# Kernel tuning notes

Measured on AMD Instinct MI355X. Metric: run time of the kernel, lower is better.

The kernel has to match this reference:

```python
import jax, jax.numpy as jnp
import numpy as np

B, T, D = 2, 2048, 2048
H, HD = 16, 128
ROPE_BASE = 10000.0
EPS = 1e-6


def setup_inputs() -> dict:
    key = jax.random.key(0)
    ks = jax.random.split(key, 5)
    s = 1.0 / np.sqrt(D)
    return {
        "x": jax.random.normal(ks[0], (B, T, D), dtype=jnp.float32),
        "Wq": jax.random.normal(ks[1], (H * HD, D), dtype=jnp.float32) * s,
        "Wk": jax.random.normal(ks[2], (H * HD, D), dtype=jnp.float32) * s,
        "Wv": jax.random.normal(ks[3], (H * HD, D), dtype=jnp.float32) * s,
        "Wo": jax.random.normal(ks[4], (D, H * HD), dtype=jnp.float32) * s,
        "q_norm_w": jnp.ones((HD,), dtype=jnp.float32),
        "k_norm_w": jnp.ones((HD,), dtype=jnp.float32),
    }


def _rms_norm(x, w):
    # RMSNorm over last dim, no centering (LLaMA/Qwen style)
    norm = jnp.sqrt(jnp.mean(jnp.square(x), axis=-1, keepdims=True) + EPS)
    return x / norm * w


def _rope_interleaved(x):
    # x: (B, T, H, HD); GPT-NeoX interleaved style, sequential positions
    dim = HD // 2
    freqs = jnp.exp(-jnp.arange(0, dim, dtype=jnp.float32) * jnp.log(ROPE_BASE) / dim)
    angles = jnp.arange(T, dtype=jnp.float32)[:, None] * freqs[None, :]  # (T, dim)
    cos = jnp.cos(angles)[None, :, None, :]  # (1, T, 1, dim)
    sin = jnp.sin(angles)[None, :, None, :]
    x_even = x[..., ::2]
    x_odd = x[..., 1::2]
    r_even = x_even * cos - x_odd * sin
    r_odd = x_even * sin + x_odd * cos
    return jnp.stack([r_even, r_odd], axis=-1).reshape(x.shape)


def reference(x, Wq, Wk, Wv, Wo, q_norm_w, k_norm_w):
    # QKV projections (weights stored [out, in], per llm_linear einsum)
    q = jnp.einsum("btd,od->bto", x, Wq).reshape(B, T, H, HD)
    k = jnp.einsum("btd,od->bto", x, Wk).reshape(B, T, H, HD)
    v = jnp.einsum("btd,od->bto", x, Wv).reshape(B, T, H, HD)
    # per-head QK RMSNorm
    q = _rms_norm(q, q_norm_w)
    k = _rms_norm(k, k_norm_w)
    # rotary embeddings
    q = _rope_interleaved(q)
    k = _rope_interleaved(k)
    # causal scaled dot-product attention
    scale = 1.0 / jnp.sqrt(jnp.asarray(HD, dtype=x.dtype))
    scores = jnp.einsum("bthd,bshd->bhts", q, k) * scale  # (B, H, T, T)
    causal = jnp.tril(jnp.ones((T, T), dtype=bool))
    scores = jnp.where(causal[None, None, :, :], scores, jnp.asarray(-1e30, dtype=scores.dtype))
    probs = jax.nn.softmax(scores, axis=-1)
    ctx = jnp.einsum("bhts,bshd->bthd", probs, v).reshape(B, T, H * HD)
    # output projection
    return jnp.einsum("bto,do->btd", ctx, Wo)
```

## Files before the change

### kernel.cpp

```cpp
#include <hip/hip_runtime.h>
#include <cstdint>
#include <cstddef>

#define B_ 2
#define T_ 2048
#define D_ 2048
#define H_ 16
#define HD_ 128
#define EPS_ 1e-6f
#define QSCALE_ 0.08838834764831845f
#define KVSTRIDE_ (H_ * HD_)

typedef unsigned short u16;
typedef short s16x8 __attribute__((ext_vector_type(8)));
typedef float f32x4 __attribute__((ext_vector_type(4)));

__device__ __forceinline__ float bf2f(u16 h) {
  union { unsigned int u; float f; } v;
  v.u = ((unsigned int)h) << 16;
  return v.f;
}
__device__ __forceinline__ u16 f2bf(float f) {
  union { float f; unsigned int u; } v;
  v.f = f;
  unsigned int r = v.u + 0x7FFFu + ((v.u >> 16) & 1u);
  return (u16)(r >> 16);
}

__device__ __forceinline__ void gload16(const void* g, void* l) {
  __builtin_amdgcn_global_load_lds(
      (const __attribute__((address_space(1))) unsigned int*)g,
      (__attribute__((address_space(3))) unsigned int*)l, 16, 0, 0);
}

__global__ void cvt_f32_bf16(const float* __restrict__ in, u16* __restrict__ out, int n4) {
  int i = blockIdx.x * blockDim.x + threadIdx.x;
  if (i < n4) {
    float4 v = ((const float4*)in)[i];
    ((ushort4*)out)[i] = make_ushort4(f2bf(v.x), f2bf(v.y), f2bf(v.z), f2bf(v.w));
  }
}

template <int OUT_BF16>
__global__ __launch_bounds__(256, 2) void gemm_btn(const u16* __restrict__ A,
                                                   const u16* __restrict__ Bm,
                                                   void* __restrict__ Cout,
                                                   int M, int N, int K) {
  __shared__ u16 As[2 * 128 * 32];
  __shared__ u16 Bs[2 * 128 * 32];
  const int tid = threadIdx.x;
  const int w = tid >> 6, lane = tid & 63, quad = lane >> 4, c = lane & 15;
  const int wm = w & 1, wn = w >> 1;
  const int m0 = blockIdx.y * 128, n0 = blockIdx.x * 128;

  f32x4 acc[4][4];
#pragma unroll
  for (int i = 0; i < 4; ++i)
#pragma unroll
    for (int j = 0; j < 4; ++j) acc[i][j] = (f32x4){0.f, 0.f, 0.f, 0.f};

  for (int k0 = 0; k0 < K; k0 += 64) {
    __syncthreads();
#pragma unroll
    for (int i = 0; i < 4; ++i) {
      int chunk = (w * 4 + i) * 64 + lane;
      int kc = chunk >> 9;
      int within = chunk & 511;
      int row = within >> 2, cc = within & 3;
      gload16(A + (size_t)(m0 + row) * K + k0 + kc * 32 + cc * 8, (void*)(As + chunk * 8));
      gload16(Bm + (size_t)(n0 + row) * K + k0 + kc * 32 + cc * 8, (void*)(Bs + chunk * 8));
    }
    __syncthreads();
#pragma unroll
    for (int kc = 0; kc < 2; ++kc) {
      s16x8 af[4], bf[4];
#pragma unroll
      for (int mi = 0; mi < 4; ++mi)
        af[mi] = *(const s16x8*)(As + kc * 4096 + (wm * 64 + mi * 16 + c) * 32 + quad * 8);
#pragma unroll
      for (int ni = 0; ni < 4; ++ni)
        bf[ni] = *(const s16x8*)(Bs + kc * 4096 + (wn * 64 + ni * 16 + c) * 32 + quad * 8);
#pragma unroll
      for (int mi = 0; mi < 4; ++mi)
#pragma unroll
        for (int ni = 0; ni < 4; ++ni)
          acc[mi][ni] = __builtin_amdgcn_mfma_f32_16x16x32_bf16(af[mi], bf[ni], acc[mi][ni], 0, 0, 0);
    }
  }

#pragma unroll
  for (int mi = 0; mi < 4; ++mi)
#pragma unroll
    for (int ni = 0; ni < 4; ++ni)
#pragma unroll
      for (int r = 0; r < 4; ++r) {
        int row = m0 + wm * 64 + mi * 16 + quad * 4 + r;
        int col = n0 + wn * 64 + ni * 16 + c;
        float v = acc[mi][ni][r];
        if (OUT_BF16)
          ((u16*)Cout)[(size_t)row * N + col] = f2bf(v);
        else
          ((float*)Cout)[(size_t)row * N + col] = v;
      }
}

__global__ void rmsnorm_rope(u16* __restrict__ x, const float* __restrict__ nw, float outscale) {
  const int tid = threadIdx.x;
  const int w = tid >> 6, lane = tid & 63;
  const int vec = blockIdx.x * 4 + w;
  const int t = (vec >> 4) & (T_ - 1);
  u16* base = x + (size_t)vec * HD_;
  unsigned int pk = *(const unsigned int*)(base + lane * 2);
  float e = bf2f((u16)(pk & 0xFFFFu));
  float o = bf2f((u16)(pk >> 16));
  float ss = e * e + o * o;
#pragma unroll
  for (int off = 1; off < 64; off <<= 1) ss += __shfl_xor(ss, off, 64);
  float rn = rsqrtf(ss * (1.0f / HD_) + EPS_);
  float we = nw[lane * 2], wo = nw[lane * 2 + 1];
  e = e * rn * we;
  o = o * rn * wo;
  float freq = expf(-(float)lane * (9.210340371976184f / 64.0f));
  float ang = (float)t * freq;
  float sn, cs;
  sincosf(ang, &sn, &cs);
  float re = (e * cs - o * sn) * outscale;
  float ro = (e * sn + o * cs) * outscale;
  *(unsigned int*)(base + lane * 2) = ((unsigned int)f2bf(ro) << 16) | (unsigned int)f2bf(re);
}

__global__ __launch_bounds__(256, 2) void attn_fwd(const u16* __restrict__ Q,
                                                   const u16* __restrict__ Kg,
                                                   const u16* __restrict__ Vt,
                                                   u16* __restrict__ O) {
  __shared__ u16 Ks[2][64 * 128];
  __shared__ u16 Vts[2][128 * 64];
  __shared__ u16 Ps[64 * 64];
  const int tid = threadIdx.x;
  const int w = tid >> 6, lane = tid & 63, quad = lane >> 4, c = lane & 15;
  const int c7 = (c & 7) * 8;
  const int bid = blockIdx.x;
  const int qt = 31 - (bid >> 5);
  const int h = bid & 15;
  const int b = (bid >> 4) & 1;
  const int q0 = qt * 64;

  s16x8 qf[4];
  const u16* qbase = Q + ((size_t)(b * T_ + q0 + w * 16 + c) * H_ + h) * HD_;
#pragma unroll
  for (int kk = 0; kk < 4; ++kk) qf[kk] = *(const s16x8*)(qbase + kk * 32 + quad * 8);

  f32x4 of[8];
#pragma unroll
  for (int i = 0; i < 8; ++i) of[i] = (f32x4){0.f, 0.f, 0.f, 0.f};
  float m_i[4] = {-1e30f, -1e30f, -1e30f, -1e30f};
  float lp[4] = {0.f, 0.f, 0.f, 0.f};

  const u16* kbase = Kg + ((size_t)b * T_ * H_ + h) * HD_;
  const u16* vtbase = Vt + (size_t)(h * HD_) * (B_ * T_) + (size_t)b * T_;

  auto STAGE = [&](int j, int buf) {
    const u16* krow = kbase + (size_t)(j * 64) * KVSTRIDE_;
    const u16* vrow = vtbase + j * 64;
#pragma unroll
    for (int i = 0; i < 4; ++i) {
      int chunk = i * 256 + tid;
      int krowi = chunk >> 4, kslot = (chunk & 15) ^ (krowi & 7);
      gload16(krow + (size_t)krowi * KVSTRIDE_ + kslot * 8, (void*)(&Ks[buf][0] + chunk * 8));
      int vrowi = chunk >> 3, vslot = (chunk & 7) ^ (vrowi & 7);
      gload16(vrow + (size_t)vrowi * (B_ * T_) + vslot * 8, (void*)(&Vts[buf][0] + chunk * 8));
    }
  };

  STAGE(0, 0);
  __syncthreads();
  int cur = 0;

  for (int j = 0; j <= qt; ++j) {
    if (j < qt) STAGE(j + 1, cur ^ 1);

    f32x4 sf[4];
#pragma unroll
    for (int ni = 0; ni < 4; ++ni) {
      f32x4 a = (f32x4){0.f, 0.f, 0.f, 0.f};
#pragma unroll
      for (int kk = 0; kk < 4; ++kk) {
        s16x8 bfr = *(const s16x8*)(&Ks[cur][(ni * 16 + c) * 128 + ((kk * 32 + quad * 8) ^ c7)]);
        a = __builtin_amdgcn_mfma_f32_16x16x32_bf16(qf[kk], bfr, a, 0, 0, 0);
      }
      sf[ni] = a;
    }
    if (j == qt) {
#pragma unroll
      for (int ni = 0; ni < 4; ++ni)
#pragma unroll
        for (int r = 0; r < 4; ++r) {
          int rowg = w * 16 + quad * 4 + r;
          int colg = ni * 16 + c;
          if (colg > rowg) sf[ni][r] = -1e30f;
        }
    }
    float mc[4];
#pragma unroll
    for (int r = 0; r < 4; ++r)
      mc[r] = fmaxf(fmaxf(sf[0][r], sf[1][r]), fmaxf(sf[2][r], sf[3][r]));
#pragma unroll
    for (int off = 1; off < 16; off <<= 1)
#pragma unroll
      for (int r = 0; r < 4; ++r) mc[r] = fmaxf(mc[r], __shfl_xor(mc[r], off, 64));
#pragma unroll
    for (int r = 0; r < 4; ++r) {
      float mnew = fmaxf(m_i[r], mc[r]);
      float alpha = __expf(m_i[r] - mnew);
      m_i[r] = mnew;
      lp[r] *= alpha;
#pragma unroll
      for (int ot = 0; ot < 8; ++ot) of[ot][r] *= alpha;
    }
#pragma unroll
    for (int ni = 0; ni < 4; ++ni)
#pragma unroll
      for (int r = 0; r < 4; ++r) {
        float p = __expf(sf[ni][r] - m_i[r]);
        sf[ni][r] = p;
        lp[r] += p;
      }
#pragma unroll
    for (int ni = 0; ni < 4; ++ni)
#pragma unroll
      for (int r = 0; r < 4; ++r) {
        int row = w * 16 + quad * 4 + r;
        Ps[row * 64 + ((ni * 16 + c) ^ ((row & 7) * 8))] = f2bf(sf[ni][r]);
      }
    s16x8 pa[2];
    pa[0] = *(const s16x8*)(&Ps[(w * 16 + c) * 64 + ((quad * 8) ^ c7)]);
    pa[1] = *(const s16x8*)(&Ps[(w * 16 + c) * 64 + ((32 + quad * 8) ^ c7)]);
#pragma unroll
    for (int ot = 0; ot < 8; ++ot) {
#pragma unroll
      for (int kk = 0; kk < 2; ++kk) {
        s16x8 vfr = *(const s16x8*)(&Vts[cur][(ot * 16 + c) * 64 + ((kk * 32 + quad * 8) ^ c7)]);
        of[ot] = __builtin_amdgcn_mfma_f32_16x16x32_bf16(pa[kk], vfr, of[ot], 0, 0, 0);
      }
    }

    __syncthreads();
    cur ^= 1;
  }

#pragma unroll
  for (int off = 1; off < 16; off <<= 1)
#pragma unroll
    for (int r = 0; r < 4; ++r) lp[r] += __shfl_xor(lp[r], off, 64);
  float inv[4];
#pragma unroll
  for (int r = 0; r < 4; ++r) inv[r] = 1.0f / lp[r];
  u16* obase = O + ((size_t)(b * T_ + q0) * H_ + h) * HD_;
#pragma unroll
  for (int ot = 0; ot < 8; ++ot)
#pragma unroll
    for (int r = 0; r < 4; ++r)
      obase[(size_t)(w * 16 + quad * 4 + r) * KVSTRIDE_ + ot * 16 + c] = f2bf(of[ot][r] * inv[r]);
}

extern "C" void kernel_launch(void* const* d_in, const int* in_sizes, int n_in,
                              void* d_out, int out_size, void* d_ws, size_t ws_size,
                              hipStream_t stream) {
  const float* x = (const float*)d_in[0];
  const float* Wq = (const float*)d_in[1];
  const float* Wk = (const float*)d_in[2];
  const float* Wv = (const float*)d_in[3];
  const float* Wo = (const float*)d_in[4];
  const float* qw = (const float*)d_in[5];
  const float* kw = (const float*)d_in[6];
  float* out = (float*)d_out;

  const size_t xE = (size_t)B_ * T_ * D_;
  const size_t wE = (size_t)D_ * H_ * HD_;
  const size_t need = xE * 2 * 5 + wE * 2 * 4;
  if (ws_size < need) return;

  char* ws = (char*)d_ws;
  u16* xb = (u16*)ws;   ws += xE * 2;
  u16* wqb = (u16*)ws;  ws += wE * 2;
  u16* wkb = (u16*)ws;  ws += wE * 2;
  u16* wvb = (u16*)ws;  ws += wE * 2;
  u16* wob = (u16*)ws;  ws += wE * 2;
  u16* qb = (u16*)ws;   ws += xE * 2;
  u16* kb = (u16*)ws;   ws += xE * 2;
  u16* vtb = (u16*)ws;  ws += xE * 2;
  u16* ctxb = (u16*)ws; ws += xE * 2;

  cvt_f32_bf16<<<xE / 1024, 256, 0, stream>>>(x, xb, (int)(xE / 4));
  cvt_f32_bf16<<<wE / 1024, 256, 0, stream>>>(Wq, wqb, (int)(wE / 4));
  cvt_f32_bf16<<<wE / 1024, 256, 0, stream>>>(Wk, wkb, (int)(wE / 4));
  cvt_f32_bf16<<<wE / 1024, 256, 0, stream>>>(Wv, wvb, (int)(wE / 4));
  cvt_f32_bf16<<<wE / 1024, 256, 0, stream>>>(Wo, wob, (int)(wE / 4));

  dim3 gg(16, 32);
  gemm_btn<1><<<gg, 256, 0, stream>>>(xb, wqb, qb, 4096, 2048, 2048);
  gemm_btn<1><<<gg, 256, 0, stream>>>(xb, wkb, kb, 4096, 2048, 2048);
  dim3 ggv(32, 16);
  gemm_btn<1><<<ggv, 256, 0, stream>>>(wvb, xb, vtb, 2048, 4096, 2048);

  rmsnorm_rope<<<16384, 256, 0, stream>>>(qb, qw, QSCALE_);
  rmsnorm_rope<<<16384, 256, 0, stream>>>(kb, kw, 1.0f);

  attn_fwd<<<B_ * H_ * (T_ / 64), 256, 0, stream>>>(qb, kb, vtb, ctxb);

  gemm_btn<0><<<gg, 256, 0, stream>>>(ctxb, wob, out, 4096, 2048, 2048);
}
```

Before: 411.8 us.

## Double-buffer GEMM LDS tiles and fuse Q/K projections into one launch

The GEMM now uses two LDS buffers and prefetches the next K-tile with global_load_lds while computing MFMAs on the current one, dropping one barrier per iteration. The Q and K weights are converted into one contiguous buffer, so a single GEMM with N=4096 computes both projections and writes each half to its own output. This is meant to hide global-load latency and cut a launch while filling the GPU better. LDS use doubles to 64KB per block, which may limit occupancy under launch_bounds(256,2).

```diff
diff --git a/kernel.cpp b/kernel.cpp
--- a/kernel.cpp
+++ b/kernel.cpp
@@ -41,17 +41,19 @@
   }
 }
 
-template <int OUT_BF16>
+template <int MODE>
 __global__ __launch_bounds__(256, 2) void gemm_btn(const u16* __restrict__ A,
                                                    const u16* __restrict__ Bm,
                                                    void* __restrict__ Cout,
+                                                   void* __restrict__ Cout2,
                                                    int M, int N, int K) {
-  __shared__ u16 As[2 * 128 * 32];
-  __shared__ u16 Bs[2 * 128 * 32];
+  __shared__ u16 As[2][2 * 128 * 32];
+  __shared__ u16 Bs[2][2 * 128 * 32];
   const int tid = threadIdx.x;
   const int w = tid >> 6, lane = tid & 63, quad = lane >> 4, c = lane & 15;
   const int wm = w & 1, wn = w >> 1;
   const int m0 = blockIdx.y * 128, n0 = blockIdx.x * 128;
+  const int NT = K >> 6;
 
   f32x4 acc[4][4];
 #pragma unroll
@@ -59,35 +61,54 @@
 #pragma unroll
     for (int j = 0; j < 4; ++j) acc[i][j] = (f32x4){0.f, 0.f, 0.f, 0.f};
 
-  for (int k0 = 0; k0 < K; k0 += 64) {
-    __syncthreads();
+  auto STAGE = [&](int t, int buf) {
+    int k0 = t << 6;
 #pragma unroll
     for (int i = 0; i < 4; ++i) {
       int chunk = (w * 4 + i) * 64 + lane;
       int kc = chunk >> 9;
       int within = chunk & 511;
       int row = within >> 2, cc = within & 3;
-      gload16(A + (size_t)(m0 + row) * K + k0 + kc * 32 + cc * 8, (void*)(As + chunk * 8));
-      gload16(Bm + (size_t)(n0 + row) * K + k0 + kc * 32 + cc * 8, (void*)(Bs + chunk * 8));
-    }
+      gload16(A + (size_t)(m0 + row) * K + k0 + kc * 32 + cc * 8, (void*)(&As[buf][0] + chunk * 8));
+      gload16(Bm + (size_t)(n0 + row) * K + k0 + kc * 32 + cc * 8, (void*)(&Bs[buf][0] + chunk * 8));
+    }
+  };
+
+  STAGE(0, 0);
+  __syncthreads();
+  int cur = 0;
+
+  for (int t = 0; t < NT; ++t) {
+    if (t + 1 < NT) STAGE(t + 1, cur ^ 1);
+
+    s16x8 af[4][2], bf[4][2];
+#pragma unroll
+    for (int kc = 0; kc < 2; ++kc) {
+#pragma unroll
+      for (int mi = 0; mi < 4; ++mi)
+        af[mi][kc] = *(const s16x8*)(&As[cur][0] + kc * 4096 + (wm * 64 + mi * 16 + c) * 32 + quad * 8);
+#pragma unroll
+      for (int ni = 0; ni < 4; ++ni)
+        bf[ni][kc] = *(const s16x8*)(&Bs[cur][0] + kc * 4096 + (wn * 64 + ni * 16 + c) * 32 + quad * 8);
+    }
+#pragma unroll
+    for (int kc = 0; kc < 2; ++kc)
+#pragma unroll
+      for (int mi = 0; mi < 4; ++mi)
+#pragma unroll
+        for (int ni = 0; ni < 4; ++ni)
+          acc[mi][ni] = __builtin_amdgcn_mfma_f32_16x16x32_bf16(af[mi][kc], bf[ni][kc], acc[mi][ni], 0, 0, 0);
+
     __syncthreads();
-#pragma unroll
-    for (int kc = 0; kc < 2; ++kc) {
-      s16x8 af[4], bf[4];
-#pragma unroll
-      for (int mi = 0; mi < 4; ++mi)
-        af[mi] = *(const s16x8*)(As + kc * 4096 + (wm * 64 + mi * 16 + c) * 32 + quad * 8);
-#pragma unroll
-      for (int ni = 0; ni < 4; ++ni)
-        bf[ni] = *(const s16x8*)(Bs + kc * 4096 + (wn * 64 + ni * 16 + c) * 32 + quad * 8);
-#pragma unroll
-      for (int mi = 0; mi < 4; ++mi)
-#pragma unroll
-        for (int ni = 0; ni < 4; ++ni)
-          acc[mi][ni] = __builtin_amdgcn_mfma_f32_16x16x32_bf16(af[mi], bf[ni], acc[mi][ni], 0, 0, 0);
-    }
+    cur ^= 1;
   }
 
+  u16* dst16 = (u16*)Cout;
+  int coloff = 0, nstride = N;
+  if (MODE == 2) {
+    nstride = 2048;
+    if (n0 >= 2048) { dst16 = (u16*)Cout2; coloff = -2048; }
+  }
 #pragma unroll
   for (int mi = 0; mi < 4; ++mi)
 #pragma unroll
@@ -95,12 +116,12 @@
 #pragma unroll
       for (int r = 0; r < 4; ++r) {
         int row = m0 + wm * 64 + mi * 16 + quad * 4 + r;
-        int col = n0 + wn * 64 + ni * 16 + c;
+        int col = n0 + wn * 64 + ni * 16 + c + coloff;
         float v = acc[mi][ni][r];
-        if (OUT_BF16)
-          ((u16*)Cout)[(size_t)row * N + col] = f2bf(v);
+        if (MODE == 0)
+          ((float*)Cout)[(size_t)row * N + col] = v;
         else
-          ((float*)Cout)[(size_t)row * N + col] = v;
+          dst16[(size_t)row * nstride + col] = f2bf(v);
       }
 }
 
@@ -281,32 +302,31 @@
   if (ws_size < need) return;
 
   char* ws = (char*)d_ws;
-  u16* xb = (u16*)ws;   ws += xE * 2;
-  u16* wqb = (u16*)ws;  ws += wE * 2;
-  u16* wkb = (u16*)ws;  ws += wE * 2;
-  u16* wvb = (u16*)ws;  ws += wE * 2;
-  u16* wob = (u16*)ws;  ws += wE * 2;
-  u16* qb = (u16*)ws;   ws += xE * 2;
-  u16* kb = (u16*)ws;   ws += xE * 2;
-  u16* vtb = (u16*)ws;  ws += xE * 2;
-  u16* ctxb = (u16*)ws; ws += xE * 2;
+  u16* xb = (u16*)ws;    ws += xE * 2;
+  u16* wqkb = (u16*)ws;  ws += wE * 2 * 2;
+  u16* wvb = (u16*)ws;   ws += wE * 2;
+  u16* wob = (u16*)ws;   ws += wE * 2;
+  u16* qb = (u16*)ws;    ws += xE * 2;
+  u16* kb = (u16*)ws;    ws += xE * 2;
+  u16* vtb = (u16*)ws;   ws += xE * 2;
+  u16* ctxb = (u16*)ws;  ws += xE * 2;
 
   cvt_f32_bf16<<<xE / 1024, 256, 0, stream>>>(x, xb, (int)(xE / 4));
-  cvt_f32_bf16<<<wE / 1024, 256, 0, stream>>>(Wq, wqb, (int)(wE / 4));
-  cvt_f32_bf16<<<wE / 1024, 256, 0, stream>>>(Wk, wkb, (int)(wE / 4));
+  cvt_f32_bf16<<<wE / 1024, 256, 0, stream>>>(Wq, wqkb, (int)(wE / 4));
+  cvt_f32_bf16<<<wE / 1024, 256, 0, stream>>>(Wk, wqkb + wE, (int)(wE / 4));
   cvt_f32_bf16<<<wE / 1024, 256, 0, stream>>>(Wv, wvb, (int)(wE / 4));
   cvt_f32_bf16<<<wE / 1024, 256, 0, stream>>>(Wo, wob, (int)(wE / 4));
 
-  dim3 gg(16, 32);
-  gemm_btn<1><<<gg, 256, 0, stream>>>(xb, wqb, qb, 4096, 2048, 2048);
-  gemm_btn<1><<<gg, 256, 0, stream>>>(xb, wkb, kb, 4096, 2048, 2048);
+  dim3 gqk(32, 32);
+  gemm_btn<2><<<gqk, 256, 0, stream>>>(xb, wqkb, qb, kb, 4096, 4096, 2048);
   dim3 ggv(32, 16);
-  gemm_btn<1><<<ggv, 256, 0, stream>>>(wvb, xb, vtb, 2048, 4096, 2048);
+  gemm_btn<1><<<ggv, 256, 0, stream>>>(wvb, xb, vtb, nullptr, 2048, 4096, 2048);
 
   rmsnorm_rope<<<16384, 256, 0, stream>>>(qb, qw, QSCALE_);
   rmsnorm_rope<<<16384, 256, 0, stream>>>(kb, kw, 1.0f);
 
   attn_fwd<<<B_ * H_ * (T_ / 64), 256, 0, stream>>>(qb, kb, vtb, ctxb);
 
-  gemm_btn<0><<<gg, 256, 0, stream>>>(ctxb, wob, out, 4096, 2048, 2048);
-}
+  dim3 gg(16, 32);
+  gemm_btn<0><<<gg, 256, 0, stream>>>(ctxb, wob, out, nullptr, 4096, 2048, 2048);
+}
```

Result: faster. 397.8 us (-3.4%).
